# Performance work log

Hardware: AMD Instinct MI355X
Metric: run time of the kernel (lower is better)

Reference implementation:

```python
import jax, jax.numpy as jnp
import numpy as np

DIM = 2048
NUM_EXPERTS = 64
TOP_K = 2
IMPORTANCE_COEFF = 0.1
LOAD_COEFF = 0.1
EPS = 1e-09
N_TOKENS = 16384


def setup_inputs() -> dict:
    key = jax.random.key(0)
    k1, k2, k3, k4 = jax.random.split(key, 4)
    x = jax.random.normal(k1, (N_TOKENS, DIM), dtype=jnp.float32)
    noise = jax.random.normal(k2, (N_TOKENS, NUM_EXPERTS), dtype=jnp.float32)
    # Learned router weights (module zero-inits; we use small random for a non-degenerate baseline)
    W_gate = jax.random.normal(k3, (NUM_EXPERTS, DIM), dtype=jnp.float32) * 0.02
    W_noise = jax.random.normal(k4, (NUM_EXPERTS, DIM), dtype=jnp.float32) * 0.02
    return {"x": x, "noise": noise, "W_gate": W_gate, "W_noise": W_noise}


def _cv_squared(v, eps=EPS):
    mean = v.mean()
    var = jnp.mean((v - mean) ** 2)
    return var / (mean * mean + eps)


def _phi(z):
    # standard normal CDF
    return 0.5 * (1.0 + jax.lax.erf(z / jnp.sqrt(jnp.float32(2.0))))


def reference(x, noise, W_gate, W_noise):
    N = x.shape[0]
    k = TOP_K
    logits = x @ W_gate.T                                  # [N, E]
    noise_std = jax.nn.softplus(x @ W_noise.T) + EPS       # [N, E]
    noisy_logits = logits + noise * noise_std              # training-mode noise injection

    topv, topi = jax.lax.top_k(noisy_logits, k)            # [N, k]
    rows = jnp.arange(N)[:, None]
    masked = jnp.full_like(noisy_logits, -jnp.inf).at[rows, topi].set(topv)
    gates_full = jax.nn.softmax(masked, axis=-1)           # [N, E]
    weights = jnp.take_along_axis(gates_full, topi, axis=1)  # [N, k]
    priority = weights.max(axis=-1)                        # [N]

    # importance loss
    importance = gates_full.sum(axis=0)                    # [E]
    aux = IMPORTANCE_COEFF * _cv_squared(importance)

    # load loss (prob each expert is in top-k under the noise model)
    tv, ti = jax.lax.top_k(noisy_logits, k + 1)            # [N, k+1]
    v_k = tv[:, k - 1]
    v_kplus = tv[:, k]
    in_topk = jnp.zeros((N, NUM_EXPERTS), dtype=bool).at[rows, ti[:, :k]].set(True)
    kth_excl = jnp.where(in_topk, v_kplus[:, None], v_k[:, None])  # [N, E]
    z = (logits - kth_excl) / (noise_std + EPS)
    load = _phi(z).sum(axis=0)                             # [E]
    aux = aux + LOAD_COEFF * _cv_squared(load)

    return topi, weights, priority, aux
```

## Files before the change

### kernel.cpp

```cpp
#include <hip/hip_runtime.h>
#include <hip/hip_bf16.h>
#include <float.h>
#include <math.h>

#define N_TOK 16384
#define DIM   2048
#define NE    64
#define ROWS  128
#define TB    32
#define KT    64
#define KTP   68
#define EPSF  1e-9f

__device__ __forceinline__ float wave_sum(float v) {
#pragma unroll
    for (int d = 32; d > 0; d >>= 1) v += __shfl_xor(v, d, 64);
    return v;
}

__device__ __forceinline__ void wave_argmax(float v, int i, float& mv, int& mi) {
    float bv = v; int bi = i;
#pragma unroll
    for (int d = 32; d > 0; d >>= 1) {
        float ov = __shfl_xor(bv, d, 64);
        int   oi = __shfl_xor(bi, d, 64);
        if (ov > bv || (ov == bv && oi < bi)) { bv = ov; bi = oi; }
    }
    mv = bv; mi = bi;
}

__global__ __launch_bounds__(256, 2) void router_kernel(
    const float* __restrict__ x,
    const float* __restrict__ noise,
    const float* __restrict__ Wg,
    const float* __restrict__ Wn,
    float* __restrict__ out,
    float* __restrict__ accum)
{
    __shared__ float xs[TB][KTP];
    __shared__ float wsh[ROWS][KTP];
    __shared__ float logi[TB][ROWS + 1];
    __shared__ float s_part[4][2][NE];

    const int t  = threadIdx.x;
    const int og = t & 15;
    const int tg = t >> 4;
    const int tokBase = blockIdx.x * TB;

    float acc[2][8];
#pragma unroll
    for (int i = 0; i < 2; ++i)
#pragma unroll
        for (int j = 0; j < 8; ++j) acc[i][j] = 0.f;

    for (int k0 = 0; k0 < DIM; k0 += KT) {
#pragma unroll
        for (int r = 0; r < 2; ++r) {
            int idx = t + 256 * r;
            int row = idx >> 4, c4 = idx & 15;
            float4 v = *(const float4*)(x + (size_t)(tokBase + row) * DIM + k0 + c4 * 4);
            *(float4*)&xs[row][c4 * 4] = v;
        }
#pragma unroll
        for (int r = 0; r < 8; ++r) {
            int idx = t + 256 * r;
            int row = idx >> 4, c4 = idx & 15;
            const float* src = (row < NE) ? (Wg + (size_t)row * DIM)
                                          : (Wn + (size_t)(row - NE) * DIM);
            float4 v = *(const float4*)(src + k0 + c4 * 4);
            *(float4*)&wsh[row][c4 * 4] = v;
        }
        __syncthreads();

#pragma unroll 4
        for (int kk4 = 0; kk4 < KT / 4; ++kk4) {
            float4 xv[2], wv[8];
#pragma unroll
            for (int i = 0; i < 2; ++i)
                xv[i] = *(const float4*)&xs[tg + 16 * i][kk4 * 4];
#pragma unroll
            for (int j = 0; j < 8; ++j)
                wv[j] = *(const float4*)&wsh[og + 16 * j][kk4 * 4];
#pragma unroll
            for (int i = 0; i < 2; ++i)
#pragma unroll
                for (int j = 0; j < 8; ++j) {
                    acc[i][j] += xv[i].x * wv[j].x;
                    acc[i][j] += xv[i].y * wv[j].y;
                    acc[i][j] += xv[i].z * wv[j].z;
                    acc[i][j] += xv[i].w * wv[j].w;
                }
        }
        __syncthreads();
    }

#pragma unroll
    for (int i = 0; i < 2; ++i)
#pragma unroll
        for (int j = 0; j < 8; ++j)
            logi[tg + 16 * i][og + 16 * j] = acc[i][j];
    __syncthreads();

    const int wv_id = t >> 6;
    const int lane  = t & 63;
    float imp_acc = 0.f, load_acc = 0.f;

    for (int tt = 0; tt < TB / 4; ++tt) {
        const int tok = wv_id * (TB / 4) + tt;
        const int gt  = tokBase + tok;

        float logit = logi[tok][lane];
        float rawn  = logi[tok][NE + lane];
        float sp   = fmaxf(rawn, 0.f) + log1pf(expf(-fabsf(rawn)));
        float nstd = sp + EPSF;
        float nz   = noise[(size_t)gt * NE + lane];
        float noisy = logit + nz * nstd;

        float v0, v1, v2; int i0, i1, i2d;
        wave_argmax(noisy, lane, v0, i0);
        float m1 = (lane == i0) ? -FLT_MAX : noisy;
        wave_argmax(m1, lane, v1, i1);
        float m2 = (lane == i0 || lane == i1) ? -FLT_MAX : noisy;
        wave_argmax(m2, lane, v2, i2d);
        (void)i2d;

        float e1 = expf(v1 - v0);
        float den = 1.f + e1;
        float w0v = 1.f / den;
        float w1v = e1 / den;

        if (lane == 0) {
            out[2 * gt]                 = (float)i0;
            out[2 * gt + 1]             = (float)i1;
            out[2 * N_TOK + 2 * gt]     = w0v;
            out[2 * N_TOK + 2 * gt + 1] = w1v;
            out[4 * N_TOK + gt]         = w0v;
        }

        imp_acc += (lane == i0) ? w0v : ((lane == i1) ? w1v : 0.f);

        bool in_topk = (lane == i0) || (lane == i1);
        float kth = in_topk ? v2 : v1;
        float z = (logit - kth) / (nstd + EPSF);
        load_acc += 0.5f * (1.f + erff(z * 0.7071067811865476f));
    }

    s_part[wv_id][0][lane] = imp_acc;
    s_part[wv_id][1][lane] = load_acc;
    __syncthreads();

    if (t < 2 * NE) {
        int which = t >> 6, e = t & 63;
        float s = s_part[0][which][e] + s_part[1][which][e]
                + s_part[2][which][e] + s_part[3][which][e];
        atomicAdd(&accum[which * NE + e], s);
    }
}

__global__ void finalize_kernel(const float* __restrict__ accum,
                                float* __restrict__ out_aux) {
    const int lane = threadIdx.x;
    float imp  = accum[lane];
    float load = accum[NE + lane];

    float m_imp = wave_sum(imp) * (1.f / NE);
    float di = imp - m_imp;
    float var_imp = wave_sum(di * di) * (1.f / NE);

    float m_load = wave_sum(load) * (1.f / NE);
    float dl = load - m_load;
    float var_load = wave_sum(dl * dl) * (1.f / NE);

    if (lane == 0) {
        out_aux[0] = 0.1f * (var_imp  / (m_imp  * m_imp  + EPSF))
                   + 0.1f * (var_load / (m_load * m_load + EPSF));
    }
}

extern "C" void kernel_launch(void* const* d_in, const int* in_sizes, int n_in,
                              void* d_out, int out_size, void* d_ws, size_t ws_size,
                              hipStream_t stream) {
    const float* x     = (const float*)d_in[0];
    const float* noise = (const float*)d_in[1];
    const float* Wg    = (const float*)d_in[2];
    const float* Wn    = (const float*)d_in[3];
    float* out   = (float*)d_out;
    float* accum = (float*)d_ws;

    hipMemsetAsync(d_ws, 0, 2 * NE * sizeof(float), stream);
    router_kernel<<<N_TOK / TB, 256, 0, stream>>>(x, noise, Wg, Wn, out, accum);
    finalize_kernel<<<1, 64, 0, stream>>>(accum, out + 5 * (size_t)N_TOK);
}
```

Measured before the change: 344.6 us.

## Enlarge token tile, split K across half-blocks, prefetch x into registers

Doubles the tokens per block to 64 and has each half of the block (128 threads) compute the full 64x128 logit tile over one half of the reduction dimension, with an 8x8 register tile per thread, then sums the two halves through shared memory. The next x tile is prefetched into registers while the current one is computed. The goal is to raise arithmetic intensity per shared-memory load, halve how often the weight matrix is reloaded, and hide global load latency. In exchange, register pressure rises (launch bounds drop to one block per SM), and there are only 256 blocks, which could leave the GPU underfilled.

```diff
diff --git a/kernel.cpp b/kernel.cpp
--- a/kernel.cpp
+++ b/kernel.cpp
@@ -7,10 +7,16 @@
 #define DIM   2048
 #define NE    64
 #define ROWS  128
-#define TB    32
+#define TB    64
 #define KT    64
+#define KHALF 1024
+#define NKT   16
 #define KTP   68
 #define EPSF  1e-9f
+
+#define XS_OFF(h)   ((h) * (TB * KTP))
+#define WS_OFF(h)   (2 * TB * KTP + (h) * (ROWS * KTP))
+#define SM_FLOATS   (2 * TB * KTP + 2 * ROWS * KTP)
 
 __device__ __forceinline__ float wave_sum(float v) {
 #pragma unroll
@@ -29,7 +35,7 @@
     mv = bv; mi = bi;
 }
 
-__global__ __launch_bounds__(256, 2) void router_kernel(
+__global__ __launch_bounds__(256, 1) void router_kernel(
     const float* __restrict__ x,
     const float* __restrict__ noise,
     const float* __restrict__ Wg,
@@ -37,52 +43,71 @@
     float* __restrict__ out,
     float* __restrict__ accum)
 {
-    __shared__ float xs[TB][KTP];
-    __shared__ float wsh[ROWS][KTP];
-    __shared__ float logi[TB][ROWS + 1];
-    __shared__ float s_part[4][2][NE];
-
-    const int t  = threadIdx.x;
-    const int og = t & 15;
-    const int tg = t >> 4;
+    __shared__ float sm[SM_FLOATS];
+
+    const int t   = threadIdx.x;
+    const int kz  = t >> 7;
+    const int u   = t & 127;
+    const int tg  = u >> 4;
+    const int og  = u & 15;
+    const int c4  = t & 15;
+    const int rs  = t >> 4;
     const int tokBase = blockIdx.x * TB;
 
-    float acc[2][8];
-#pragma unroll
-    for (int i = 0; i < 2; ++i)
+    float acc[8][8];
+#pragma unroll
+    for (int i = 0; i < 8; ++i)
 #pragma unroll
         for (int j = 0; j < 8; ++j) acc[i][j] = 0.f;
 
-    for (int k0 = 0; k0 < DIM; k0 += KT) {
-#pragma unroll
-        for (int r = 0; r < 2; ++r) {
-            int idx = t + 256 * r;
-            int row = idx >> 4, c4 = idx & 15;
-            float4 v = *(const float4*)(x + (size_t)(tokBase + row) * DIM + k0 + c4 * 4);
-            *(float4*)&xs[row][c4 * 4] = v;
-        }
+    float4 px[8];
+#pragma unroll
+    for (int r = 0; r < 8; ++r) {
+        int row = (rs + 16 * r) & 63;
+        int h   = r >> 2;
+        px[r] = *(const float4*)(x + (size_t)(tokBase + row) * DIM + h * KHALF + c4 * 4);
+    }
+
+    for (int kt = 0; kt < NKT; ++kt) {
+        __syncthreads();
 #pragma unroll
         for (int r = 0; r < 8; ++r) {
-            int idx = t + 256 * r;
-            int row = idx >> 4, c4 = idx & 15;
-            const float* src = (row < NE) ? (Wg + (size_t)row * DIM)
-                                          : (Wn + (size_t)(row - NE) * DIM);
-            float4 v = *(const float4*)(src + k0 + c4 * 4);
-            *(float4*)&wsh[row][c4 * 4] = v;
+            int row = (rs + 16 * r) & 63;
+            int h   = r >> 2;
+            *(float4*)(sm + XS_OFF(h) + row * KTP + c4 * 4) = px[r];
+        }
+#pragma unroll
+        for (int r = 0; r < 16; ++r) {
+            int wrow = (rs + 16 * r) & 127;
+            int h    = r >> 3;
+            const float* src = (wrow < NE) ? (Wg + (size_t)wrow * DIM)
+                                           : (Wn + (size_t)(wrow - NE) * DIM);
+            float4 v = *(const float4*)(src + h * KHALF + kt * KT + c4 * 4);
+            *(float4*)(sm + WS_OFF(h) + wrow * KTP + c4 * 4) = v;
         }
         __syncthreads();
-
+        if (kt < NKT - 1) {
+#pragma unroll
+            for (int r = 0; r < 8; ++r) {
+                int row = (rs + 16 * r) & 63;
+                int h   = r >> 2;
+                px[r] = *(const float4*)(x + (size_t)(tokBase + row) * DIM
+                                           + h * KHALF + (kt + 1) * KT + c4 * 4);
+            }
+        }
+        const float* xb = sm + XS_OFF(kz);
+        const float* wb = sm + WS_OFF(kz);
 #pragma unroll 4
         for (int kk4 = 0; kk4 < KT / 4; ++kk4) {
-            float4 xv[2], wv[8];
-#pragma unroll
-            for (int i = 0; i < 2; ++i)
-                xv[i] = *(const float4*)&xs[tg + 16 * i][kk4 * 4];
+            float4 xv[8], wv[8];
+#pragma unroll
+            for (int i = 0; i < 8; ++i)
+                xv[i] = *(const float4*)(xb + (tg + 8 * i) * KTP + kk4 * 4);
 #pragma unroll
             for (int j = 0; j < 8; ++j)
-                wv[j] = *(const float4*)&wsh[og + 16 * j][kk4 * 4];
-#pragma unroll
-            for (int i = 0; i < 2; ++i)
+                wv[j] = *(const float4*)(wb + (og + 16 * j) * KTP + kk4 * 4);
+#pragma unroll
+            for (int i = 0; i < 8; ++i)
 #pragma unroll
                 for (int j = 0; j < 8; ++j) {
                     acc[i][j] += xv[i].x * wv[j].x;
@@ -91,14 +116,26 @@
                     acc[i][j] += xv[i].w * wv[j].w;
                 }
         }
-        __syncthreads();
-    }
-
-#pragma unroll
-    for (int i = 0; i < 2; ++i)
-#pragma unroll
-        for (int j = 0; j < 8; ++j)
-            logi[tg + 16 * i][og + 16 * j] = acc[i][j];
+    }
+
+    __syncthreads();
+    float* logi   = sm;
+    float* s_part = sm + TB * (ROWS + 1);
+    if (kz == 0) {
+#pragma unroll
+        for (int i = 0; i < 8; ++i)
+#pragma unroll
+            for (int j = 0; j < 8; ++j)
+                logi[(tg + 8 * i) * (ROWS + 1) + og + 16 * j] = acc[i][j];
+    }
+    __syncthreads();
+    if (kz == 1) {
+#pragma unroll
+        for (int i = 0; i < 8; ++i)
+#pragma unroll
+            for (int j = 0; j < 8; ++j)
+                logi[(tg + 8 * i) * (ROWS + 1) + og + 16 * j] += acc[i][j];
+    }
     __syncthreads();
 
     const int wv_id = t >> 6;
@@ -109,8 +146,8 @@
         const int tok = wv_id * (TB / 4) + tt;
         const int gt  = tokBase + tok;
 
-        float logit = logi[tok][lane];
-        float rawn  = logi[tok][NE + lane];
+        float logit = logi[tok * (ROWS + 1) + lane];
+        float rawn  = logi[tok * (ROWS + 1) + NE + lane];
         float sp   = fmaxf(rawn, 0.f) + log1pf(expf(-fabsf(rawn)));
         float nstd = sp + EPSF;
         float nz   = noise[(size_t)gt * NE + lane];
@@ -124,7 +161,7 @@
         wave_argmax(m2, lane, v2, i2d);
         (void)i2d;
 
-        float e1 = expf(v1 - v0);
+        float e1  = expf(v1 - v0);
         float den = 1.f + e1;
         float w0v = 1.f / den;
         float w1v = e1 / den;
@@ -145,14 +182,14 @@
         load_acc += 0.5f * (1.f + erff(z * 0.7071067811865476f));
     }
 
-    s_part[wv_id][0][lane] = imp_acc;
-    s_part[wv_id][1][lane] = load_acc;
+    s_part[(wv_id * 2 + 0) * NE + lane] = imp_acc;
+    s_part[(wv_id * 2 + 1) * NE + lane] = load_acc;
     __syncthreads();
 
     if (t < 2 * NE) {
         int which = t >> 6, e = t & 63;
-        float s = s_part[0][which][e] + s_part[1][which][e]
-                + s_part[2][which][e] + s_part[3][which][e];
+        float s = s_part[(0 * 2 + which) * NE + e] + s_part[(1 * 2 + which) * NE + e]
+                + s_part[(2 * 2 + which) * NE + e] + s_part[(3 * 2 + which) * NE + e];
         atomicAdd(&accum[which * NE + e], s);
     }
 }
```

After: 367.3 us. 6.6% more time.

## Split router into split-K GEMM kernel with register prefetch and separate epilogue

Applied to the files above, without the earlier changes.

The fused router kernel is split into two kernels. A GEMM kernel runs 1024 workgroups, each computing a 64-token by 64-expert tile for one of the two weight matrices over half of the K dimension. It prefetches the next K tile through registers and uses a swizzled block order, then writes partial logits to a workspace. A separate epilogue kernel adds the two K partials and does softplus, top-k, softmax and the loss accumulation. This aims for more parallelism and better latency hiding. The cost is an extra launch and a global round trip for the partial logits. x is now read twice (once per weight half), though the split halves likely share it through L2.

```diff
diff --git a/kernel.cpp b/kernel.cpp
--- a/kernel.cpp
+++ b/kernel.cpp
@@ -6,10 +6,10 @@
 #define N_TOK 16384
 #define DIM   2048
 #define NE    64
-#define ROWS  128
-#define TB    32
-#define KT    64
-#define KTP   68
+#define KH    1024
+#define KT    32
+#define NKT   32
+#define KTP   36
 #define EPSF  1e-9f
 
 __device__ __forceinline__ float wave_sum(float v) {
@@ -29,60 +29,71 @@
     mv = bv; mi = bi;
 }
 
-__global__ __launch_bounds__(256, 2) void router_kernel(
+__global__ __launch_bounds__(128, 2) void gemm64_kernel(
     const float* __restrict__ x,
-    const float* __restrict__ noise,
     const float* __restrict__ Wg,
     const float* __restrict__ Wn,
-    float* __restrict__ out,
-    float* __restrict__ accum)
+    float* __restrict__ P)
 {
-    __shared__ float xs[TB][KTP];
-    __shared__ float wsh[ROWS][KTP];
-    __shared__ float logi[TB][ROWS + 1];
-    __shared__ float s_part[4][2][NE];
-
-    const int t  = threadIdx.x;
-    const int og = t & 15;
-    const int tg = t >> 4;
-    const int tokBase = blockIdx.x * TB;
-
-    float acc[2][8];
-#pragma unroll
-    for (int i = 0; i < 2; ++i)
+    __shared__ float xs[64][KTP];
+    __shared__ float wsh[64][KTP];
+
+    const int wg   = blockIdx.x;
+    const int L    = (wg & 7) * 128 + (wg >> 3);
+    const int tt   = L >> 2;
+    const int half = (L >> 1) & 1;
+    const int ks   = L & 1;
+
+    const int t    = threadIdx.x;
+    const int f4c  = t & 7;
+    const int rowb = t >> 3;
+    const int tg   = t >> 3;
+    const int og   = t & 7;
+
+    const float* W = half ? Wn : Wg;
+    const int tokBase = tt * 64;
+    const int kbase   = ks * KH;
+
+    float acc[4][8];
+#pragma unroll
+    for (int i = 0; i < 4; ++i)
 #pragma unroll
         for (int j = 0; j < 8; ++j) acc[i][j] = 0.f;
 
-    for (int k0 = 0; k0 < DIM; k0 += KT) {
-#pragma unroll
-        for (int r = 0; r < 2; ++r) {
-            int idx = t + 256 * r;
-            int row = idx >> 4, c4 = idx & 15;
-            float4 v = *(const float4*)(x + (size_t)(tokBase + row) * DIM + k0 + c4 * 4);
-            *(float4*)&xs[row][c4 * 4] = v;
-        }
-#pragma unroll
-        for (int r = 0; r < 8; ++r) {
-            int idx = t + 256 * r;
-            int row = idx >> 4, c4 = idx & 15;
-            const float* src = (row < NE) ? (Wg + (size_t)row * DIM)
-                                          : (Wn + (size_t)(row - NE) * DIM);
-            float4 v = *(const float4*)(src + k0 + c4 * 4);
-            *(float4*)&wsh[row][c4 * 4] = v;
-        }
+    float4 px[4], pw[4];
+#pragma unroll
+    for (int r = 0; r < 4; ++r) {
+        px[r] = *(const float4*)(x + (size_t)(tokBase + rowb + 16 * r) * DIM + kbase + f4c * 4);
+        pw[r] = *(const float4*)(W + (size_t)(rowb + 16 * r) * DIM + kbase + f4c * 4);
+    }
+
+    for (int kt = 0; kt < NKT; ++kt) {
         __syncthreads();
-
-#pragma unroll 4
+#pragma unroll
+        for (int r = 0; r < 4; ++r) {
+            *(float4*)&xs[rowb + 16 * r][f4c * 4]  = px[r];
+            *(float4*)&wsh[rowb + 16 * r][f4c * 4] = pw[r];
+        }
+        __syncthreads();
+        if (kt < NKT - 1) {
+            const int koff = kbase + (kt + 1) * KT;
+#pragma unroll
+            for (int r = 0; r < 4; ++r) {
+                px[r] = *(const float4*)(x + (size_t)(tokBase + rowb + 16 * r) * DIM + koff + f4c * 4);
+                pw[r] = *(const float4*)(W + (size_t)(rowb + 16 * r) * DIM + koff + f4c * 4);
+            }
+        }
+#pragma unroll
         for (int kk4 = 0; kk4 < KT / 4; ++kk4) {
-            float4 xv[2], wv[8];
-#pragma unroll
-            for (int i = 0; i < 2; ++i)
+            float4 xv[4], wv[8];
+#pragma unroll
+            for (int i = 0; i < 4; ++i)
                 xv[i] = *(const float4*)&xs[tg + 16 * i][kk4 * 4];
 #pragma unroll
             for (int j = 0; j < 8; ++j)
-                wv[j] = *(const float4*)&wsh[og + 16 * j][kk4 * 4];
-#pragma unroll
-            for (int i = 0; i < 2; ++i)
+                wv[j] = *(const float4*)&wsh[og + 8 * j][kk4 * 4];
+#pragma unroll
+            for (int i = 0; i < 4; ++i)
 #pragma unroll
                 for (int j = 0; j < 8; ++j) {
                     acc[i][j] += xv[i].x * wv[j].x;
@@ -91,29 +102,39 @@
                     acc[i][j] += xv[i].w * wv[j].w;
                 }
         }
-        __syncthreads();
-    }
-
-#pragma unroll
-    for (int i = 0; i < 2; ++i)
+    }
+
+    float* Pk = P + (size_t)ks * N_TOK * 128;
+#pragma unroll
+    for (int i = 0; i < 4; ++i)
 #pragma unroll
         for (int j = 0; j < 8; ++j)
-            logi[tg + 16 * i][og + 16 * j] = acc[i][j];
-    __syncthreads();
-
-    const int wv_id = t >> 6;
-    const int lane  = t & 63;
+            Pk[(size_t)(tokBase + tg + 16 * i) * 128 + half * 64 + og + 8 * j] = acc[i][j];
+}
+
+__global__ __launch_bounds__(256) void epilogue_kernel(
+    const float* __restrict__ P,
+    const float* __restrict__ noise,
+    float* __restrict__ out,
+    float* __restrict__ accum)
+{
+    __shared__ float s_part[4][2][NE];
+    const int t    = threadIdx.x;
+    const int wv   = t >> 6;
+    const int lane = t & 63;
+    const float* P0 = P;
+    const float* P1 = P + (size_t)N_TOK * 128;
+
     float imp_acc = 0.f, load_acc = 0.f;
 
-    for (int tt = 0; tt < TB / 4; ++tt) {
-        const int tok = wv_id * (TB / 4) + tt;
-        const int gt  = tokBase + tok;
-
-        float logit = logi[tok][lane];
-        float rawn  = logi[tok][NE + lane];
+    for (int s = 0; s < 8; ++s) {
+        const int tok = blockIdx.x * 32 + wv * 8 + s;
+
+        float logit = P0[(size_t)tok * 128 + lane]      + P1[(size_t)tok * 128 + lane];
+        float rawn  = P0[(size_t)tok * 128 + 64 + lane] + P1[(size_t)tok * 128 + 64 + lane];
         float sp   = fmaxf(rawn, 0.f) + log1pf(expf(-fabsf(rawn)));
         float nstd = sp + EPSF;
-        float nz   = noise[(size_t)gt * NE + lane];
+        float nz   = noise[(size_t)tok * NE + lane];
         float noisy = logit + nz * nstd;
 
         float v0, v1, v2; int i0, i1, i2d;
@@ -124,17 +145,17 @@
         wave_argmax(m2, lane, v2, i2d);
         (void)i2d;
 
-        float e1 = expf(v1 - v0);
+        float e1  = expf(v1 - v0);
         float den = 1.f + e1;
         float w0v = 1.f / den;
         float w1v = e1 / den;
 
         if (lane == 0) {
-            out[2 * gt]                 = (float)i0;
-            out[2 * gt + 1]             = (float)i1;
-            out[2 * N_TOK + 2 * gt]     = w0v;
-            out[2 * N_TOK + 2 * gt + 1] = w1v;
-            out[4 * N_TOK + gt]         = w0v;
+            out[2 * tok]                 = (float)i0;
+            out[2 * tok + 1]             = (float)i1;
+            out[2 * N_TOK + 2 * tok]     = w0v;
+            out[2 * N_TOK + 2 * tok + 1] = w1v;
+            out[4 * N_TOK + tok]         = w0v;
         }
 
         imp_acc += (lane == i0) ? w0v : ((lane == i1) ? w1v : 0.f);
@@ -145,8 +166,8 @@
         load_acc += 0.5f * (1.f + erff(z * 0.7071067811865476f));
     }
 
-    s_part[wv_id][0][lane] = imp_acc;
-    s_part[wv_id][1][lane] = load_acc;
+    s_part[wv][0][lane] = imp_acc;
+    s_part[wv][1][lane] = load_acc;
     __syncthreads();
 
     if (t < 2 * NE) {
@@ -186,8 +207,10 @@
     const float* Wn    = (const float*)d_in[3];
     float* out   = (float*)d_out;
     float* accum = (float*)d_ws;
-
-    hipMemsetAsync(d_ws, 0, 2 * NE * sizeof(float), stream);
-    router_kernel<<<N_TOK / TB, 256, 0, stream>>>(x, noise, Wg, Wn, out, accum);
+    float* P     = accum + 128;
+
+    hipMemsetAsync(accum, 0, 2 * NE * sizeof(float), stream);
+    gemm64_kernel<<<1024, 128, 0, stream>>>(x, Wg, Wn, P);
+    epilogue_kernel<<<N_TOK / 32, 256, 0, stream>>>(P, noise, out, accum);
     finalize_kernel<<<1, 64, 0, stream>>>(accum, out + 5 * (size_t)N_TOK);
 }
```

Measured after the change: 427.2 us. +24.0%, slower.
